# Kernel optimization log

Hardware: AMD Instinct MI355X
Metric: run time of the kernel (lower is better)

Reference implementation:

```python
import jax, jax.numpy as jnp
import numpy as np


def setup_inputs() -> dict:
    key = jax.random.key(0)
    x = jax.random.normal(key, (4096, 4096), dtype=jnp.float32)
    return {"x": x}


def reference(x):
    """IDCT (DCT-III) along the last axis, scaled by 2 as in DREAMPlace:
        out[k] = x[0] + 2 * sum_{n=1}^{N-1} x[n] * cos(pi*n*(2k+1)/(2N))
    computed via a 2N-point FFT with twiddle-factor (expk) pre-multiply.
    """
    N = x.shape[-1]
    # twiddle expk[n] = exp(j*pi*n/(2N))
    theta = (jnp.pi / (2.0 * N)) * jnp.arange(N, dtype=jnp.float32)
    expk = jax.lax.complex(jnp.cos(theta), jnp.sin(theta))  # complex64 [N]
    c = x.astype(jnp.complex64) * expk                       # [M, N]
    # zero-pad to 2N; S[k] = sum_n c[n] exp(+j*2*pi*n*k/(2N)) = conj(fft(conj(c2)))[k]
    c2 = jnp.concatenate([c, jnp.zeros_like(c)], axis=-1)    # [M, 2N]
    S = jnp.fft.fft(jnp.conj(c2))                            # Re(S) == Re(2N*ifft(c2))
    # out[k] = 2*Re(S[k]) - x[0]
    y = 2.0 * jnp.real(S[..., :N]) - x[..., :1]
    return y.astype(x.dtype)
```

## Files before the change

kernel.cpp:

```cpp
#include <hip/hip_runtime.h>
#include <stdint.h>


#define Md 4096
#define Nfull 4096
#define Ph 2048
#define Kh 2048
#define BM 128
#define BN 128
#define BK 32

typedef short bf16x8 __attribute__((ext_vector_type(8)));
typedef float floatx4 __attribute__((ext_vector_type(4)));
typedef unsigned short ushort_t;

__device__ __forceinline__ ushort_t f2bf(float f) {
  union { float f; uint32_t u; } v; v.f = f;
  uint32_t u = v.u;
  return (ushort_t)((u + 0x7fffu + ((u >> 16) & 1u)) >> 16);
}

__global__ __launch_bounds__(256) void prep_kernel(const float* __restrict__ x,
                                                   ushort_t* __restrict__ A,
                                                   ushort_t* __restrict__ Ce,
                                                   ushort_t* __restrict__ Co) {
  int b = blockIdx.x;
  if (b < 8192) {
    int i = (b * 256 + threadIdx.x) * 8;
    int m = i >> 12;
    int j = i & 4095;
    float4 a = *(const float4*)(x + i);
    float4 c = *(const float4*)(x + i + 4);
    union { ushort_t us[4]; int2 v; } ev, od;
    ev.us[0] = f2bf(a.x); od.us[0] = f2bf(a.y);
    ev.us[1] = f2bf(a.z); od.us[1] = f2bf(a.w);
    ev.us[2] = f2bf(c.x); od.us[2] = f2bf(c.y);
    ev.us[3] = f2bf(c.z); od.us[3] = f2bf(c.w);
    int half = j >> 1;
    *(int2*)(A + m * Nfull + half) = ev.v;
    *(int2*)(A + m * Nfull + Ph + half) = od.v;
  } else {
    int idx = ((b - 8192) * 256 + threadIdx.x) * 8;
    const float s = 3.14159265358979f / 8192.0f;
    union { ushort_t us[8]; int4 v; } pk;
    if (idx < Ph * Kh) {
      int p = idx >> 11;
      int ne0 = idx & 2047;
      int tp = 2 * p + 1;
#pragma unroll
      for (int jj = 0; jj < 8; ++jj) {
        int n = 2 * (ne0 + jj);
        int t = (n * tp) & 16383;
        float c = (n == 0) ? 1.0f : 2.0f * __cosf(s * (float)t);
        pk.us[jj] = f2bf(c);
      }
      *(int4*)(Ce + idx) = pk.v;
    } else {
      int local = idx - Ph * Kh;
      int p = local >> 11;
      int no0 = local & 2047;
      int tp = 2 * p + 1;
#pragma unroll
      for (int jj = 0; jj < 8; ++jj) {
        int n = 2 * (no0 + jj) + 1;
        int t = (n * tp) & 16383;
        pk.us[jj] = f2bf(2.0f * __cosf(s * (float)t));
      }
      *(int4*)(Co + local) = pk.v;
    }
  }
}

__global__ __launch_bounds__(256, 2) void gemm_fused(const ushort_t* __restrict__ A,
                                                     const ushort_t* __restrict__ Ce,
                                                     const ushort_t* __restrict__ Co,
                                                     float* __restrict__ out) {
  __shared__ __align__(16) ushort_t AsE[BM * BK];
  __shared__ __align__(16) ushort_t AsO[BM * BK];
  __shared__ __align__(16) ushort_t BsE[BN * BK];
  __shared__ __align__(16) ushort_t BsO[BN * BK];

  const int tid = threadIdx.x;
  const int wid = tid >> 6;
  const int lane = tid & 63;

  const int bm = blockIdx.y * BM;
  const int bn = blockIdx.x * BN;

  const int wm = (wid & 1) * 64;
  const int wn = (wid >> 1) * 64;

  const int lrow = lane & 15;
  const int kq = (lane >> 4) * 8;

  floatx4 accE[4][4] = {};
  floatx4 accO[4][4] = {};

  const int r0 = tid >> 2, e0 = (tid & 3) * 8;
  const int r1 = r0 + 64;
  const int l0 = wid * 512;
  const int l1 = 2048 + wid * 512;

  const ushort_t* Ae = A + (size_t)bm * Nfull;
  const ushort_t* Ao = Ae + Ph;
  const ushort_t* Be = Ce + (size_t)bn * Kh;
  const ushort_t* Bo = Co + (size_t)bn * Kh;

#define GLDS(src, dst) __builtin_amdgcn_global_load_lds( \
      (const __attribute__((address_space(1))) void*)(src), \
      (__attribute__((address_space(3))) void*)(dst), 16, 0, 0)

  for (int k0 = 0; k0 < Kh; k0 += BK) {
    GLDS(Ae + (size_t)r0 * Nfull + k0 + e0, AsE + l0);
    GLDS(Ae + (size_t)r1 * Nfull + k0 + e0, AsE + l1);
    GLDS(Ao + (size_t)r0 * Nfull + k0 + e0, AsO + l0);
    GLDS(Ao + (size_t)r1 * Nfull + k0 + e0, AsO + l1);
    GLDS(Be + (size_t)r0 * Kh + k0 + e0, BsE + l0);
    GLDS(Be + (size_t)r1 * Kh + k0 + e0, BsE + l1);
    GLDS(Bo + (size_t)r0 * Kh + k0 + e0, BsO + l0);
    GLDS(Bo + (size_t)r1 * Kh + k0 + e0, BsO + l1);
    __syncthreads();

    bf16x8 bE[4], bO[4];
#pragma unroll
    for (int f = 0; f < 4; ++f) {
      bE[f] = *(const bf16x8*)(BsE + (wn + f * 16 + lrow) * BK + kq);
      bO[f] = *(const bf16x8*)(BsO + (wn + f * 16 + lrow) * BK + kq);
    }
#pragma unroll
    for (int im = 0; im < 4; ++im) {
      bf16x8 aE = *(const bf16x8*)(AsE + (wm + im * 16 + lrow) * BK + kq);
      bf16x8 aO = *(const bf16x8*)(AsO + (wm + im * 16 + lrow) * BK + kq);
#pragma unroll
      for (int jn = 0; jn < 4; ++jn) {
        accE[im][jn] = __builtin_amdgcn_mfma_f32_16x16x32_bf16(aE, bE[jn], accE[im][jn], 0, 0, 0);
        accO[im][jn] = __builtin_amdgcn_mfma_f32_16x16x32_bf16(aO, bO[jn], accO[im][jn], 0, 0, 0);
      }
    }
    __syncthreads();
  }
#undef GLDS

#pragma unroll
  for (int im = 0; im < 4; ++im) {
    int rb = bm + wm + im * 16 + (lane >> 4) * 4;
#pragma unroll
    for (int jn = 0; jn < 4; ++jn) {
      int p = bn + wn + jn * 16 + lrow;
      float* lo = out + (size_t)rb * Nfull + p;
      float* hi = out + (size_t)rb * Nfull + (Nfull - 1 - p);
#pragma unroll
      for (int r = 0; r < 4; ++r) {
        float e = accE[im][jn][r];
        float o = accO[im][jn][r];
        lo[(size_t)r * Nfull] = e + o;
        hi[(size_t)r * Nfull] = e - o;
      }
    }
  }
}

extern "C" void kernel_launch(void* const* d_in, const int* in_sizes, int n_in,
                              void* d_out, int out_size, void* d_ws, size_t ws_size,
                              hipStream_t stream) {
  const float* x = (const float*)d_in[0];
  float* out = (float*)d_out;
  ushort_t* Axb = (ushort_t*)d_ws;
  ushort_t* Ce = Axb + (size_t)Md * Nfull;
  ushort_t* Co = Ce + (size_t)Ph * Kh;

  prep_kernel<<<12288, 256, 0, stream>>>(x, Axb, Ce, Co);

  dim3 grid(Ph / BN, Md / BM);
  gemm_fused<<<grid, 256, 0, stream>>>(Axb, Ce, Co, out);
}
```

Measured before the change: 199.0 us.

## Double-buffer LDS tiles to overlap global loads with MFMA compute

Shared-memory tiles are split into two buffers. The async global-to-LDS loads for the next K-step are now issued right after a single barrier, so they run while MFMAs consume the current buffer. This replaces the old load-sync-compute-sync pattern and drops one barrier per iteration. Per-row source pointers are precomputed and advanced by BK, removing address arithmetic from the loop. The cost is double the LDS use per block (about 64KB), which may limit how many blocks fit per CU.

```diff
diff --git a/kernel.cpp b/kernel.cpp
--- a/kernel.cpp
+++ b/kernel.cpp
@@ -9,6 +9,7 @@
 #define BM 128
 #define BN 128
 #define BK 32
+#define NK (Kh / BK)
 
 typedef short bf16x8 __attribute__((ext_vector_type(8)));
 typedef float floatx4 __attribute__((ext_vector_type(4)));
@@ -75,10 +76,10 @@
                                                      const ushort_t* __restrict__ Ce,
                                                      const ushort_t* __restrict__ Co,
                                                      float* __restrict__ out) {
-  __shared__ __align__(16) ushort_t AsE[BM * BK];
-  __shared__ __align__(16) ushort_t AsO[BM * BK];
-  __shared__ __align__(16) ushort_t BsE[BN * BK];
-  __shared__ __align__(16) ushort_t BsO[BN * BK];
+  __shared__ __align__(16) ushort_t AsE[2][BM * BK];
+  __shared__ __align__(16) ushort_t AsO[2][BM * BK];
+  __shared__ __align__(16) ushort_t BsE[2][BN * BK];
+  __shared__ __align__(16) ushort_t BsO[2][BN * BK];
 
   const int tid = threadIdx.x;
   const int wid = tid >> 6;
@@ -101,44 +102,58 @@
   const int l0 = wid * 512;
   const int l1 = 2048 + wid * 512;
 
-  const ushort_t* Ae = A + (size_t)bm * Nfull;
-  const ushort_t* Ao = Ae + Ph;
-  const ushort_t* Be = Ce + (size_t)bn * Kh;
-  const ushort_t* Bo = Co + (size_t)bn * Kh;
+  const ushort_t* pAe0 = A + (size_t)(bm + r0) * Nfull + e0;
+  const ushort_t* pAe1 = A + (size_t)(bm + r1) * Nfull + e0;
+  const ushort_t* pAo0 = pAe0 + Ph;
+  const ushort_t* pAo1 = pAe1 + Ph;
+  const ushort_t* pBe0 = Ce + (size_t)(bn + r0) * Kh + e0;
+  const ushort_t* pBe1 = Ce + (size_t)(bn + r1) * Kh + e0;
+  const ushort_t* pBo0 = Co + (size_t)(bn + r0) * Kh + e0;
+  const ushort_t* pBo1 = Co + (size_t)(bn + r1) * Kh + e0;
 
 #define GLDS(src, dst) __builtin_amdgcn_global_load_lds( \
       (const __attribute__((address_space(1))) void*)(src), \
       (__attribute__((address_space(3))) void*)(dst), 16, 0, 0)
 
-  for (int k0 = 0; k0 < Kh; k0 += BK) {
-    GLDS(Ae + (size_t)r0 * Nfull + k0 + e0, AsE + l0);
-    GLDS(Ae + (size_t)r1 * Nfull + k0 + e0, AsE + l1);
-    GLDS(Ao + (size_t)r0 * Nfull + k0 + e0, AsO + l0);
-    GLDS(Ao + (size_t)r1 * Nfull + k0 + e0, AsO + l1);
-    GLDS(Be + (size_t)r0 * Kh + k0 + e0, BsE + l0);
-    GLDS(Be + (size_t)r1 * Kh + k0 + e0, BsE + l1);
-    GLDS(Bo + (size_t)r0 * Kh + k0 + e0, BsO + l0);
-    GLDS(Bo + (size_t)r1 * Kh + k0 + e0, BsO + l1);
+#define ISSUE(buf)                      \
+  do {                                  \
+    GLDS(pAe0, AsE[buf] + l0);          \
+    GLDS(pAe1, AsE[buf] + l1);          \
+    GLDS(pAo0, AsO[buf] + l0);          \
+    GLDS(pAo1, AsO[buf] + l1);          \
+    GLDS(pBe0, BsE[buf] + l0);          \
+    GLDS(pBe1, BsE[buf] + l1);          \
+    GLDS(pBo0, BsO[buf] + l0);          \
+    GLDS(pBo1, BsO[buf] + l1);          \
+    pAe0 += BK; pAe1 += BK; pAo0 += BK; pAo1 += BK; \
+    pBe0 += BK; pBe1 += BK; pBo0 += BK; pBo1 += BK; \
+  } while (0)
+
+  ISSUE(0);
+
+  for (int k = 0; k < NK; ++k) {
+    const int b = k & 1;
     __syncthreads();
+    if (k + 1 < NK) ISSUE(b ^ 1);
 
     bf16x8 bE[4], bO[4];
 #pragma unroll
     for (int f = 0; f < 4; ++f) {
-      bE[f] = *(const bf16x8*)(BsE + (wn + f * 16 + lrow) * BK + kq);
-      bO[f] = *(const bf16x8*)(BsO + (wn + f * 16 + lrow) * BK + kq);
+      bE[f] = *(const bf16x8*)(BsE[b] + (wn + f * 16 + lrow) * BK + kq);
+      bO[f] = *(const bf16x8*)(BsO[b] + (wn + f * 16 + lrow) * BK + kq);
     }
 #pragma unroll
     for (int im = 0; im < 4; ++im) {
-      bf16x8 aE = *(const bf16x8*)(AsE + (wm + im * 16 + lrow) * BK + kq);
-      bf16x8 aO = *(const bf16x8*)(AsO + (wm + im * 16 + lrow) * BK + kq);
+      bf16x8 aE = *(const bf16x8*)(AsE[b] + (wm + im * 16 + lrow) * BK + kq);
+      bf16x8 aO = *(const bf16x8*)(AsO[b] + (wm + im * 16 + lrow) * BK + kq);
 #pragma unroll
       for (int jn = 0; jn < 4; ++jn) {
         accE[im][jn] = __builtin_amdgcn_mfma_f32_16x16x32_bf16(aE, bE[jn], accE[im][jn], 0, 0, 0);
         accO[im][jn] = __builtin_amdgcn_mfma_f32_16x16x32_bf16(aO, bO[jn], accO[im][jn], 0, 0, 0);
       }
     }
-    __syncthreads();
   }
+#undef ISSUE
 #undef GLDS
 
 #pragma unroll
```

After: 206.9 us. 1.04x slower.
